# Kernel tuning notes

Hardware: AMD Instinct MI355X
Metric: run time of the kernel (lower is better)

## Reference

```python
import jax, jax.numpy as jnp
import numpy as np

jax.config.update("jax_enable_x64", True)  # FixedPointMul math is done in float64, as in torch

B, S, H = 8, 4096, 768


def setup_inputs():
    key = jax.random.key(0)
    k = jax.random.split(key, 6)
    s_act = jnp.array([4.0 / 127.0], dtype=jnp.float32)  # per-tensor 8-bit activation scale

    def qact(kk):  # produce int8-quantized-looking activations
        x = jax.random.normal(kk, (B, S, H), jnp.float32)
        return s_act * jnp.clip(jnp.round(x / s_act), -128, 127)

    return {
        "hidden_states": qact(k[0]),
        "hidden_states_scaling_factor": s_act,
        "input_tensor": qact(k[1]),
        "input_tensor_scaling_factor": s_act,
        "dense_weight": 0.02 * jax.random.normal(k[2], (H, H), jnp.float32),
        "dense_bias": 0.01 * jax.random.normal(k[3], (H,), jnp.float32),
        "ln_weight": 1.0 + 0.05 * jax.random.normal(k[4], (H,), jnp.float32),
        "ln_bias": 0.05 * jax.random.normal(k[5], (H,), jnp.float32),
    }


def _sym_scale(k, smin, smax):
    n = 2 ** (k - 1) - 1
    return jnp.clip(jnp.maximum(jnp.abs(smin), jnp.abs(smax)), 1e-8, None) / n


def _sym_quant(x, k, scale):
    n = 2 ** (k - 1) - 1
    return jnp.clip(jnp.round(x / scale), -n, n - 1)


def _batch_frexp(x):
    # returns (round(mantissa * 2^31), 31 - exponent) as in ibert batch_frexp
    m, e = jnp.frexp(x)
    return jnp.floor(m * (2.0 ** 31) + 0.5), 31.0 - e


def _fixedpoint_mul(x, pre_scale, bit, z_scale, identity=None, id_scale=None):
    n = 2 ** (bit - 1) - 1
    ps = jnp.reshape(pre_scale, (1, 1, -1)).astype(jnp.float64)
    z = z_scale.astype(jnp.float64)
    z_int = jnp.round(x.astype(jnp.float64) / ps)
    m, e = _batch_frexp(ps / z)
    out = jnp.round(z_int * m / (2.0 ** e))
    if identity is not None:
        isf = jnp.reshape(id_scale, (1, 1, -1)).astype(jnp.float64)
        wx = jnp.round(identity.astype(jnp.float64) / isf)
        m1, e1 = _batch_frexp(isf / z)
        out = out + jnp.round(wx * m1 / (2.0 ** e1))
    return jnp.clip(out, -n - 1, n).astype(jnp.float32)


def _quant_act(x, bit, pre_scale, identity=None, id_scale=None):
    x_act = x if identity is None else x + identity
    s = _sym_scale(bit, x_act.min(), x_act.max())  # per-tensor scale (dynamic range)
    q = _fixedpoint_mul(x, pre_scale, bit, s, identity, id_scale)
    return q * s, s


def reference(hidden_states, hidden_states_scaling_factor, input_tensor, input_tensor_scaling_factor, dense_weight, dense_bias, ln_weight, ln_bias):
    # ---- QuantLinear: per-channel int8 weights, int32 bias ----
    w_min = dense_weight.min(axis=1)
    w_max = dense_weight.max(axis=1)
    fc_scale = _sym_scale(8, w_min, w_max)                      # [H_out]
    w_int = _sym_quant(dense_weight, 8, fc_scale[:, None])      # [H_out, H_in]
    bias_scale = fc_scale * hidden_states_scaling_factor        # [H_out]
    b_int = _sym_quant(dense_bias, 32, bias_scale)
    x_int = hidden_states / hidden_states_scaling_factor
    hs = (jnp.einsum("bsh,oh->bso", x_int, w_int) + b_int) * bias_scale
    # dropout: eval mode -> identity
    # ---- QuantAct(22-bit) with quantized residual add ----
    hs, ln_in_scale = _quant_act(hs, 22, bias_scale, input_tensor, input_tensor_scaling_factor)
    # ---- IntLayerNorm (integer-only LayerNorm) ----
    x_int = hs / ln_in_scale
    mean_int = jnp.round(jnp.mean(x_int, axis=2, keepdims=True))
    y_int = x_int - mean_int
    var0 = jnp.sum(y_int ** 2, axis=2, keepdims=True)
    shift = jnp.ceil(jnp.log2(jnp.sqrt(jnp.maximum(var0, 1.0) / 2.0 ** 32)))  # set_shift (max_bit=32)
    shift = jnp.maximum(0.0, shift.max())
    y_sh = jnp.floor(y_int / 2.0 ** shift)
    var_int = jnp.sum(y_sh ** 2, axis=2, keepdims=True)
    std_int = jnp.floor(jnp.sqrt(var_int)) * 2.0 ** shift
    factor = jnp.floor(2.0 ** 31 / std_int)
    y_int = jnp.floor(y_int * factor / 2.0)
    sf = jnp.sqrt(jnp.float32(H)) / 2.0 ** 30
    bias_int = jnp.floor((ln_bias / ln_weight) / sf)
    y_int = y_int + bias_int
    sf_out = sf * ln_weight                                     # [H]
    hs = y_int * sf_out
    # ---- QuantAct(8-bit) output requantization ----
    hs, out_scale = _quant_act(hs, 8, sf_out)
    return hs, out_scale
```

## Files before the change

kernel.cpp:

```cpp
#include <hip/hip_runtime.h>

typedef int   v4i   __attribute__((ext_vector_type(4)));
typedef unsigned long u64x2 __attribute__((ext_vector_type(2)));

#define HDIM 768
#define NTOK 32768

static constexpr size_t WX_OFF   = 0;
static constexpr size_t WINT_OFF = 25165824;
static constexpr size_t FACT_OFF = WINT_OFF + 589824;
static constexpr size_t RS1_OFF  = WINT_OFF + 1179648;
static constexpr size_t RS2_OFF  = RS1_OFF + 6144;
static constexpr size_t BS_OFF   = RS2_OFF + 6144;
static constexpr size_t BINT_OFF = BS_OFF + 3072;
static constexpr size_t LNBI_OFF = BINT_OFF + 3072;
static constexpr size_t SFO_OFF  = LNBI_OFF + 3072;
static constexpr size_t SC_OFF   = SFO_OFF + 3072;
static constexpr size_t RSM1_OFF = SC_OFF + 64;
static constexpr size_t INP8_OFF = RSM1_OFF + 64;
static constexpr size_t WS_NEED8 = INP8_OFF + (size_t)NTOK * HDIM;

__device__ __forceinline__ unsigned fenc(float f) {
    unsigned u = __float_as_uint(f);
    return (u >> 31) ? ~u : (u | 0x80000000u);
}
__device__ __forceinline__ float fdec(unsigned e) {
    unsigned u = (e >> 31) ? (e & 0x7fffffffu) : ~e;
    return __uint_as_float(u);
}

#define GLDS16(g, l) __builtin_amdgcn_global_load_lds( \
    (const __attribute__((address_space(1))) unsigned int*)(g), \
    (__attribute__((address_space(3))) unsigned int*)(l), 16, 0, 0)

__device__ __forceinline__ int swz4(int r) { return (r & 3) ^ ((r >> 2) & 3); }

__global__ __launch_bounds__(256) void k0_prep(const float* __restrict__ W,
                                               const float* __restrict__ bias,
                                               const float* __restrict__ ln_w,
                                               const float* __restrict__ ln_b,
                                               const float* __restrict__ phsf,
                                               char* __restrict__ ws) {
    int o = blockIdx.x, tid = threadIdx.x;
    __shared__ float red[256];
    __shared__ float fc_sh;
    float m = 0.f;
    for (int j = tid; j < HDIM; j += 256) m = fmaxf(m, fabsf(W[(size_t)o * HDIM + j]));
    red[tid] = m;
    __syncthreads();
    for (int s = 128; s; s >>= 1) { if (tid < s) red[tid] = fmaxf(red[tid], red[tid + s]); __syncthreads(); }
    if (tid == 0) {
        float fc = fmaxf(red[0], 1e-8f) / 127.0f;
        float hsf = *phsf;
        float bs = fc * hsf;
        fc_sh = fc;
        ((float*)(ws + BS_OFF))[o] = bs;
        ((int*)(ws + BINT_OFF))[o] = (int)rintf(bias[o] / bs);
        float sf = sqrtf(768.0f) / 1073741824.0f;
        float lw = ln_w[o], lb = ln_b[o];
        ((int*)(ws + LNBI_OFF))[o] = (int)floorf((lb / lw) / sf);
        ((float*)(ws + SFO_OFF))[o] = sf * lw;
    }
    __syncthreads();
    float fc = fc_sh;
    char* w8 = (char*)(ws + WINT_OFF);
    for (int j = tid; j < HDIM; j += 256) {
        float q = rintf(W[(size_t)o * HDIM + j] / fc);
        q = fminf(fmaxf(q, -127.f), 126.f);
        w8[(size_t)o * HDIM + j] = (char)q;
    }
    if (blockIdx.x == 0 && tid < 8) {
        unsigned* sc = (unsigned*)(ws + SC_OFF);
        unsigned v = 0u;
        if (tid == 0 || tid == 2) v = 0xFFFFFFFFu;
        sc[tid] = v;
    }
}

__global__ __launch_bounds__(256) void kp_a8(const float* __restrict__ hs,
                                             const float* __restrict__ phsf,
                                             char* __restrict__ ws) {
    int tid = threadIdx.x;
    size_t b4 = (size_t)blockIdx.x * 1024 + tid;
    float inv = 1.0f / *phsf;
    const float4* in4 = (const float4*)hs;
    unsigned* o32 = (unsigned*)(ws + WX_OFF);
    #pragma unroll
    for (int j = 0; j < 4; ++j) {
        float4 v = in4[b4 + j * 256];
        int q0 = (int)rintf(v.x * inv), q1 = (int)rintf(v.y * inv);
        int q2 = (int)rintf(v.z * inv), q3 = (int)rintf(v.w * inv);
        o32[b4 + j * 256] = (unsigned)(q0 & 255) | ((unsigned)(q1 & 255) << 8) |
                            ((unsigned)(q2 & 255) << 16) | ((unsigned)(q3 & 255) << 24);
    }
}

#define BM 128
#define BN 192
#define BK 64
#define NKT (HDIM / BK)
#define SROW 196
template<int U8>
__global__ __launch_bounds__(256) void k1_gemm(const float* __restrict__ inp,
                                               char* __restrict__ i8,
                                               const float* __restrict__ pisf,
                                               char* __restrict__ ws,
                                               int* __restrict__ accOut) {
    __shared__ alignas(16) char smem[40992];
    char* As0 = smem;
    char* Bs0 = smem + 16384;
    float* rmn = (float*)(smem + 40960);
    float* rmx = rmn + 4;
    int tid = threadIdx.x, lane = tid & 63, wave = tid >> 6;
    int wrow = lane & 15, g = lane >> 4;
    int bid = blockIdx.x;
    int xcd = bid & 7, slot = bid >> 3;
    int mtile = xcd * 32 + (slot >> 2);
    int ntile = slot & 3;
    int t0 = mtile * BM, o0 = ntile * BN;
    const char* a8 = (const char*)(ws + WX_OFF);
    const char* w8 = (const char*)(ws + WINT_OFF);

    const char* asrc[2]; const char* bsrc[3];
    int aldso[2], bldso[3];
    #pragma unroll
    for (int i = 0; i < 2; ++i) {
        int c = i * 256 + tid, r = c >> 2, s = c & 3;
        asrc[i] = a8 + (size_t)(t0 + r) * HDIM + (s ^ swz4(r)) * 16;
        aldso[i] = (i * 256 + wave * 64) * 16;
    }
    #pragma unroll
    for (int i = 0; i < 3; ++i) {
        int c = i * 256 + tid, r = c >> 2, s = c & 3;
        bsrc[i] = w8 + (size_t)(o0 + r) * HDIM + (s ^ swz4(r)) * 16;
        bldso[i] = (i * 256 + wave * 64) * 16;
    }

    int wm = wave & 1, wn = wave >> 1;
    int aofs[4], bofs[6];
    #pragma unroll
    for (int mi = 0; mi < 4; ++mi) { int r = wm * 64 + mi * 16 + wrow; aofs[mi] = r * BK + ((g ^ swz4(r)) * 16); }
    #pragma unroll
    for (int nf = 0; nf < 6; ++nf) { int r = wn * 96 + nf * 16 + wrow; bofs[nf] = r * BK + ((g ^ swz4(r)) * 16); }

    #pragma unroll
    for (int i = 0; i < 2; ++i) GLDS16(asrc[i], As0 + aldso[i]);
    #pragma unroll
    for (int i = 0; i < 3; ++i) GLDS16(bsrc[i], Bs0 + bldso[i]);
    #pragma unroll
    for (int i = 0; i < 2; ++i) GLDS16(asrc[i] + BK, As0 + 8192 + aldso[i]);
    #pragma unroll
    for (int i = 0; i < 3; ++i) GLDS16(bsrc[i] + BK, Bs0 + 12288 + bldso[i]);
    asm volatile("s_waitcnt vmcnt(5)" ::: "memory");
    __builtin_amdgcn_s_barrier();

    v4i acc[4][6] = {};
    for (int kt = 0; kt < NKT; ++kt) {
        int cur = kt & 1;
        const char* Ac = As0 + cur * 8192;
        const char* Bc = Bs0 + cur * 12288;
        u64x2 af[4], bf[6];
        #pragma unroll
        for (int mi = 0; mi < 4; ++mi) af[mi] = *(const u64x2*)(Ac + aofs[mi]);
        #pragma unroll
        for (int nf = 0; nf < 6; ++nf) bf[nf] = *(const u64x2*)(Bc + bofs[nf]);
        asm volatile("s_waitcnt lgkmcnt(0)" ::: "memory");
        __builtin_amdgcn_s_barrier();
        if (kt + 2 < NKT) {
            #pragma unroll
            for (int i = 0; i < 2; ++i) GLDS16(asrc[i] + (kt + 2) * BK, As0 + cur * 8192 + aldso[i]);
            #pragma unroll
            for (int i = 0; i < 3; ++i) GLDS16(bsrc[i] + (kt + 2) * BK, Bs0 + cur * 12288 + bldso[i]);
        }
        __builtin_amdgcn_s_setprio(1);
        #pragma unroll
        for (int mi = 0; mi < 4; ++mi)
            #pragma unroll
            for (int nf = 0; nf < 6; ++nf) {
                acc[mi][nf] = __builtin_amdgcn_mfma_i32_16x16x32_i8((long)af[mi][0], (long)bf[nf][0], acc[mi][nf], 0, 0, 0);
                acc[mi][nf] = __builtin_amdgcn_mfma_i32_16x16x32_i8((long)af[mi][1], (long)bf[nf][1], acc[mi][nf], 0, 0, 0);
            }
        __builtin_amdgcn_s_setprio(0);
        if (kt + 2 < NKT) {
            asm volatile("s_waitcnt vmcnt(5)" ::: "memory");
            __builtin_amdgcn_s_barrier();
        } else if (kt + 2 == NKT) {
            asm volatile("s_waitcnt vmcnt(0)" ::: "memory");
            __builtin_amdgcn_s_barrier();
        }
    }

    const float* bscale = (const float*)(ws + BS_OFF);
    const int* bint = (const int*)(ws + BINT_OFF);
    float inv_isf = U8 ? (1.0f / *pisf) : 0.f;
    int* sAcc = (int*)smem;
    float lmn = 3.402823466e38f, lmx = -3.402823466e38f;
    #pragma unroll
    for (int mi = 0; mi < 4; ++mi) {
        __syncthreads();
        #pragma unroll
        for (int nf = 0; nf < 6; ++nf)
            #pragma unroll
            for (int r = 0; r < 4; ++r)
                sAcc[(wm * 16 + g * 4 + r) * SROW + wn * 96 + nf * 16 + wrow] = acc[mi][nf][r];
        __syncthreads();
        #pragma unroll
        for (int k = 0; k < 6; ++k) {
            int i4 = tid + k * 256;
            int sr = i4 / 48, c4 = i4 - sr * 48;
            int t = t0 + (sr >> 4) * 64 + mi * 16 + (sr & 15);
            int col = o0 + c4 * 4;
            int4 a4 = *(const int4*)&sAcc[sr * SROW + c4 * 4];
            int4 b4 = *(const int4*)&bint[col];
            float4 bs4 = *(const float4*)&bscale[col];
            a4.x += b4.x; a4.y += b4.y; a4.z += b4.z; a4.w += b4.w;
            size_t idx = (size_t)t * HDIM + col;
            *(int4*)&accOut[idx] = a4;
            float4 x4 = *(const float4*)&inp[idx];
            if (U8) {
                int w0 = (int)rintf(x4.x * inv_isf), w1 = (int)rintf(x4.y * inv_isf);
                int w2 = (int)rintf(x4.z * inv_isf), w3 = (int)rintf(x4.w * inv_isf);
                *(unsigned*)(i8 + idx) = (unsigned)(w0 & 255) | ((unsigned)(w1 & 255) << 8) |
                                         ((unsigned)(w2 & 255) << 16) | ((unsigned)(w3 & 255) << 24);
            }
            float xa;
            xa = (float)a4.x * bs4.x + x4.x; lmn = fminf(lmn, xa); lmx = fmaxf(lmx, xa);
            xa = (float)a4.y * bs4.y + x4.y; lmn = fminf(lmn, xa); lmx = fmaxf(lmx, xa);
            xa = (float)a4.z * bs4.z + x4.z; lmn = fminf(lmn, xa); lmx = fmaxf(lmx, xa);
            xa = (float)a4.w * bs4.w + x4.w; lmn = fminf(lmn, xa); lmx = fmaxf(lmx, xa);
        }
    }
    #pragma unroll
    for (int off = 32; off; off >>= 1) {
        lmn = fminf(lmn, __shfl_down(lmn, off));
        lmx = fmaxf(lmx, __shfl_down(lmx, off));
    }
    __syncthreads();
    if (lane == 0) { rmn[wave] = lmn; rmx[wave] = lmx; }
    __syncthreads();
    if (tid == 0) {
        float mn = fminf(fminf(rmn[0], rmn[1]), fminf(rmn[2], rmn[3]));
        float mx = fmaxf(fmaxf(rmx[0], rmx[1]), fmaxf(rmx[2], rmx[3]));
        volatile unsigned* sc = (volatile unsigned*)(ws + SC_OFF);
        unsigned emn = fenc(mn), emx = fenc(mx);
        if (emn < sc[0]) atomicMin((unsigned*)&sc[0], emn);
        if (emx > sc[1]) atomicMax((unsigned*)&sc[1], emx);
    }
}

__global__ __launch_bounds__(256) void k2_scale1(const float* __restrict__ pisf, char* __restrict__ ws) {
    __shared__ float s_sh;
    unsigned* sc = (unsigned*)(ws + SC_OFF);
    if (threadIdx.x == 0) {
        float mn = fdec(sc[0]), mx = fdec(sc[1]);
        float s = fmaxf(fmaxf(fabsf(mn), fabsf(mx)), 1e-8f) / 2097151.0f;
        ((float*)sc)[5] = s;
        s_sh = s;
        double r = (double)(*pisf) / (double)s;
        int ex; double mant = frexp(r, &ex);
        double m1 = floor(mant * 2147483648.0 + 0.5);
        ((double*)(ws + RSM1_OFF))[0] = m1 * exp2((double)(ex - 31));
    }
    __syncthreads();
    float s = s_sh;
    const float* bs = (const float*)(ws + BS_OFF);
    double* rs1 = (double*)(ws + RS1_OFF);
    for (int o = threadIdx.x; o < HDIM; o += 256) {
        double r = (double)bs[o] / (double)s;
        int ex; double mant = frexp(r, &ex);
        double m = floor(mant * 2147483648.0 + 0.5);
        rs1[o] = m * exp2((double)(ex - 31));
    }
}

template<int U8>
__global__ __launch_bounds__(256) void k3_rows(char* __restrict__ ws, int* __restrict__ buf,
                                               const float* __restrict__ inp,
                                               const char* __restrict__ i8,
                                               const float* __restrict__ pisf) {
    int tid = threadIdx.x, lane = tid & 63, wave = tid >> 6;
    int wid = blockIdx.x * 4 + wave;
    const double* rs1 = (const double*)(ws + RS1_OFF);
    double rsm1 = *(const double*)(ws + RSM1_OFF);
    float inv_isf = 1.0f / *pisf;
    double t_rs1[12];
    #pragma unroll
    for (int c = 0; c < 3; ++c) {
        int o0 = (lane + 64 * c) * 4;
        #pragma unroll
        for (int j = 0; j < 4; ++j) t_rs1[c * 4 + j] = rs1[o0 + j];
    }
    int localShift = 0;
    int4 aP[3]; float4 xP[3]; int wP[3];
    {
        size_t b0 = (size_t)(wid * 4) * HDIM;
        #pragma unroll
        for (int c = 0; c < 3; ++c) {
            aP[c] = ((const int4*)(buf + b0))[lane + 64 * c];
            if (U8) wP[c] = ((const int*)(i8 + b0))[lane + 64 * c];
            else    xP[c] = ((const float4*)(inp + b0))[lane + 64 * c];
        }
    }
    for (int rr = 0; rr < 4; ++rr) {
        int4 aN[3]; float4 xN[3]; int wN[3];
        if (rr < 3) {
            size_t nb = (size_t)(wid * 4 + rr + 1) * HDIM;
            #pragma unroll
            for (int c = 0; c < 3; ++c) {
                aN[c] = ((const int4*)(buf + nb))[lane + 64 * c];
                if (U8) wN[c] = ((const int*)(i8 + nb))[lane + 64 * c];
                else    xN[c] = ((const float4*)(inp + nb))[lane + 64 * c];
            }
        }
        size_t base = (size_t)(wid * 4 + rr) * HDIM;
        int q[12];
        int sum = 0;
        #pragma unroll
        for (int c = 0; c < 3; ++c) {
            int av[4] = {aP[c].x, aP[c].y, aP[c].z, aP[c].w};
            #pragma unroll
            for (int j = 0; j < 4; ++j) {
                double q1 = rint((double)av[j] * t_rs1[c * 4 + j]);
                int wxj;
                if (U8) wxj = (int)(char)(wP[c] >> (8 * j));
                else {
                    float xv = (j == 0) ? xP[c].x : (j == 1) ? xP[c].y : (j == 2) ? xP[c].z : xP[c].w;
                    wxj = (int)rintf(xv * inv_isf);
                }
                double qq = q1 + rint((double)wxj * rsm1);
                qq = fmin(fmax(qq, -2097152.0), 2097151.0);
                q[c * 4 + j] = (int)qq;
                sum += q[c * 4 + j];
            }
        }
        #pragma unroll
        for (int off = 32; off; off >>= 1) sum += __shfl_xor(sum, off);
        int mean = (int)rint((double)sum / 768.0);
        long long var0 = 0;
        #pragma unroll
        for (int k = 0; k < 12; ++k) { q[k] -= mean; var0 += (long long)q[k] * (long long)q[k]; }
        #pragma unroll
        for (int off = 32; off; off >>= 1) var0 += __shfl_xor(var0, off);
        #pragma unroll
        for (int c = 0; c < 3; ++c) {
            int4 y = {q[c * 4 + 0], q[c * 4 + 1], q[c * 4 + 2], q[c * 4 + 3]};
            ((int4*)(buf + base))[lane + 64 * c] = y;
        }
        if (lane == 0) {
            double v = (double)(var0 < 1 ? 1LL : var0);
            int sr = (int)ceil(0.5 * log2(v) - 16.0);
            localShift = max(localShift, sr);
        }
        #pragma unroll
        for (int c = 0; c < 3; ++c) { aP[c] = aN[c]; xP[c] = xN[c]; wP[c] = wN[c]; }
    }
    if (lane == 0 && localShift > 0) {
        int* sp = (int*)(ws + SC_OFF) + 4;
        if (localShift > *(volatile int*)sp) atomicMax(sp, localShift);
    }
}

__global__ __launch_bounds__(256) void k4_rows(char* __restrict__ ws, const int* __restrict__ buf) {
    int tid = threadIdx.x, lane = tid & 63, wave = tid >> 6;
    int wid = blockIdx.x * 4 + wave;
    int shift = *(((const int*)(ws + SC_OFF)) + 4);
    const int* lnbi = (const int*)(ws + LNBI_OFF);
    const float* sfo = (const float*)(ws + SFO_OFF);
    __shared__ float rmn[4], rmx[4];
    int t_lnbi[12]; float t_sfo[12];
    #pragma unroll
    for (int c = 0; c < 3; ++c) {
        int o0 = (lane + 64 * c) * 4;
        #pragma unroll
        for (int j = 0; j < 4; ++j) { t_lnbi[c * 4 + j] = lnbi[o0 + j]; t_sfo[c * 4 + j] = sfo[o0 + j]; }
    }
    unsigned* fact = (unsigned*)(ws + FACT_OFF);
    float lmn = 3.402823466e38f, lmx = -3.402823466e38f;
    int4 yP[3];
    {
        size_t b0 = (size_t)(wid * 4) * HDIM;
        #pragma unroll
        for (int c = 0; c < 3; ++c) yP[c] = ((const int4*)(buf + b0))[lane + 64 * c];
    }
    for (int rr = 0; rr < 4; ++rr) {
        int4 yN[3];
        if (rr < 3) {
            size_t nb = (size_t)(wid * 4 + rr + 1) * HDIM;
            #pragma unroll
            for (int c = 0; c < 3; ++c) yN[c] = ((const int4*)(buf + nb))[lane + 64 * c];
        }
        int yv[12];
        #pragma unroll
        for (int c = 0; c < 3; ++c) {
            yv[c * 4 + 0] = yP[c].x; yv[c * 4 + 1] = yP[c].y; yv[c * 4 + 2] = yP[c].z; yv[c * 4 + 3] = yP[c].w;
        }
        long long var = 0;
        #pragma unroll
        for (int k = 0; k < 12; ++k) { int ysh = yv[k] >> shift; var += (long long)ysh * (long long)ysh; }
        #pragma unroll
        for (int off = 32; off; off >>= 1) var += __shfl_xor(var, off);
        double std_int = floor(sqrt((double)var)) * (double)(1LL << shift);
        if (std_int < 1.0) std_int = 1.0;
        long long factor = (long long)floor(2147483648.0 / std_int);
        if (lane == 0) fact[wid * 4 + rr] = (unsigned)factor;
        #pragma unroll
        for (int k = 0; k < 12; ++k) {
            long long t = ((long long)yv[k] * factor) >> 1;
            int v2 = (int)t + t_lnbi[k];
            float h = (float)v2 * t_sfo[k];
            lmn = fminf(lmn, h);
            lmx = fmaxf(lmx, h);
        }
        #pragma unroll
        for (int c = 0; c < 3; ++c) yP[c] = yN[c];
    }
    #pragma unroll
    for (int off = 32; off; off >>= 1) {
        lmn = fminf(lmn, __shfl_xor(lmn, off));
        lmx = fmaxf(lmx, __shfl_xor(lmx, off));
    }
    if (lane == 0) { rmn[wave] = lmn; rmx[wave] = lmx; }
    __syncthreads();
    if (tid == 0) {
        float mn = fminf(fminf(rmn[0], rmn[1]), fminf(rmn[2], rmn[3]));
        float mx = fmaxf(fmaxf(rmx[0], rmx[1]), fmaxf(rmx[2], rmx[3]));
        volatile unsigned* sc = (volatile unsigned*)(ws + SC_OFF);
        unsigned emn = fenc(mn), emx = fenc(mx);
        if (emn < sc[2]) atomicMin((unsigned*)&sc[2], emn);
        if (emx > sc[3]) atomicMax((unsigned*)&sc[3], emx);
    }
}

__global__ __launch_bounds__(256) void k5_scale2(char* __restrict__ ws) {
    __shared__ float s_sh;
    unsigned* sc = (unsigned*)(ws + SC_OFF);
    if (threadIdx.x == 0) {
        float mn = fdec(sc[2]), mx = fdec(sc[3]);
        float s2 = fmaxf(fmaxf(fabsf(mn), fabsf(mx)), 1e-8f) / 127.0f;
        ((float*)sc)[6] = s2;
        s_sh = s2;
    }
    __syncthreads();
    float s2 = s_sh;
    const float* sfo = (const float*)(ws + SFO_OFF);
    double* rs2 = (double*)(ws + RS2_OFF);
    for (int o = threadIdx.x; o < HDIM; o += 256) {
        double r = (double)sfo[o] / (double)s2;
        int ex; double mant = frexp(r, &ex);
        double m = floor(mant * 2147483648.0 + 0.5);
        rs2[o] = m * exp2((double)(ex - 31));
    }
}

__global__ __launch_bounds__(256) void k6_out(char* __restrict__ ws, float* __restrict__ out) {
    int tid = threadIdx.x, lane = tid & 63, wave = tid >> 6;
    int wid = blockIdx.x * 4 + wave;
    const double* rs2 = (const double*)(ws + RS2_OFF);
    const int* lnbi = (const int*)(ws + LNBI_OFF);
    const unsigned* fact = (const unsigned*)(ws + FACT_OFF);
    float s2 = ((const float*)(ws + SC_OFF))[6];
    double t_rs2[12]; int t_lnbi[12];
    #pragma unroll
    for (int c = 0; c < 3; ++c) {
        int o0 = (lane + 64 * c) * 4;
        #pragma unroll
        for (int j = 0; j < 4; ++j) { t_rs2[c * 4 + j] = rs2[o0 + j]; t_lnbi[c * 4 + j] = lnbi[o0 + j]; }
    }
    int* buf = (int*)out;
    int4 yP[3];
    {
        size_t b0 = (size_t)(wid * 4) * HDIM;
        #pragma unroll
        for (int c = 0; c < 3; ++c) yP[c] = ((const int4*)(buf + b0))[lane + 64 * c];
    }
    for (int rr = 0; rr < 4; ++rr) {
        int4 yN[3];
        if (rr < 3) {
            size_t nb = (size_t)(wid * 4 + rr + 1) * HDIM;
            #pragma unroll
            for (int c = 0; c < 3; ++c) yN[c] = ((const int4*)(buf + nb))[lane + 64 * c];
        }
        size_t base = (size_t)(wid * 4 + rr) * HDIM;
        long long factor = (long long)fact[wid * 4 + rr];
        int yv[12];
        #pragma unroll
        for (int c = 0; c < 3; ++c) {
            yv[c * 4 + 0] = yP[c].x; yv[c * 4 + 1] = yP[c].y; yv[c * 4 + 2] = yP[c].z; yv[c * 4 + 3] = yP[c].w;
        }
        #pragma unroll
        for (int c = 0; c < 3; ++c) {
            float4 r;
            float* rp = &r.x;
            #pragma unroll
            for (int j = 0; j < 4; ++j) {
                int k = c * 4 + j;
                long long t = ((long long)yv[k] * factor) >> 1;
                int v2 = (int)t + t_lnbi[k];
                double q = rint((double)v2 * t_rs2[k]);
                q = fmin(fmax(q, -128.0), 127.0);
                rp[j] = (float)q * s2;
            }
            ((float4*)(out + base))[lane + 64 * c] = r;
        }
        #pragma unroll
        for (int c = 0; c < 3; ++c) yP[c] = yN[c];
    }
    if (wid == 0 && tid == 0) out[(size_t)NTOK * HDIM] = s2;
}

extern "C" void kernel_launch(void* const* d_in, const int* in_sizes, int n_in,
                              void* d_out, int out_size, void* d_ws, size_t ws_size,
                              hipStream_t stream) {
    const float* hs   = (const float*)d_in[0];
    const float* phsf = (const float*)d_in[1];
    const float* inp  = (const float*)d_in[2];
    const float* pisf = (const float*)d_in[3];
    const float* W    = (const float*)d_in[4];
    const float* bias = (const float*)d_in[5];
    const float* ln_w = (const float*)d_in[6];
    const float* ln_b = (const float*)d_in[7];
    char* ws = (char*)d_ws;
    float* out = (float*)d_out;
    int* buf = (int*)d_out;
    char* i8 = ws + INP8_OFF;
    bool use8 = ws_size >= WS_NEED8;

    k0_prep<<<HDIM, 256, 0, stream>>>(W, bias, ln_w, ln_b, phsf, ws);
    kp_a8<<<NTOK * HDIM / 4096, 256, 0, stream>>>(hs, phsf, ws);
    if (use8) {
        k1_gemm<1><<<(NTOK / BM) * (HDIM / BN), 256, 0, stream>>>(inp, i8, pisf, ws, buf);
        k2_scale1<<<1, 256, 0, stream>>>(pisf, ws);
        k3_rows<1><<<NTOK / 16, 256, 0, stream>>>(ws, buf, inp, i8, pisf);
    } else {
        k1_gemm<0><<<(NTOK / BM) * (HDIM / BN), 256, 0, stream>>>(inp, i8, pisf, ws, buf);
        k2_scale1<<<1, 256, 0, stream>>>(pisf, ws);
        k3_rows<0><<<NTOK / 16, 256, 0, stream>>>(ws, buf, inp, i8, pisf);
    }
    k4_rows<<<NTOK / 16, 256, 0, stream>>>(ws, buf);
    k5_scale2<<<1, 256, 0, stream>>>(ws);
    k6_out<<<NTOK / 16, 256, 0, stream>>>(ws, out);
}
```

Baseline: 431.5 us.

## Shrink GEMM N-tile to 128 and pre-quantize residual input in separate pass

The GEMM tile changes from 128x192 to 128x128, giving six N-tiles per M-tile, less shared memory, and launch bounds of 3 blocks per CU for higher occupancy. Quantizing the residual input to int8 moves from the GEMM epilogue into a new standalone kernel, and the epilogue now reads the int8 residual and dequantizes it instead of reading fp32. This adds a full extra pass over the fp32 input but cuts epilogue traffic and register pressure. The smaller tile also re-reads the activation tile more often across N-tiles.

```diff
diff --git a/kernel.cpp b/kernel.cpp
--- a/kernel.cpp
+++ b/kernel.cpp
@@ -95,94 +95,107 @@
     }
 }
 
+__global__ __launch_bounds__(256) void kp_i8(const float* __restrict__ inp,
+                                             const float* __restrict__ pisf,
+                                             char* __restrict__ ws) {
+    int tid = threadIdx.x;
+    size_t b4 = (size_t)blockIdx.x * 1024 + tid;
+    float inv = 1.0f / *pisf;
+    const float4* in4 = (const float4*)inp;
+    unsigned* o32 = (unsigned*)(ws + INP8_OFF);
+    #pragma unroll
+    for (int j = 0; j < 4; ++j) {
+        float4 v = in4[b4 + j * 256];
+        int q0 = (int)rintf(v.x * inv), q1 = (int)rintf(v.y * inv);
+        int q2 = (int)rintf(v.z * inv), q3 = (int)rintf(v.w * inv);
+        o32[b4 + j * 256] = (unsigned)(q0 & 255) | ((unsigned)(q1 & 255) << 8) |
+                            ((unsigned)(q2 & 255) << 16) | ((unsigned)(q3 & 255) << 24);
+    }
+}
+
 #define BM 128
-#define BN 192
+#define BN 128
 #define BK 64
 #define NKT (HDIM / BK)
-#define SROW 196
+#define SROW 132
 template<int U8>
-__global__ __launch_bounds__(256) void k1_gemm(const float* __restrict__ inp,
-                                               char* __restrict__ i8,
-                                               const float* __restrict__ pisf,
-                                               char* __restrict__ ws,
-                                               int* __restrict__ accOut) {
-    __shared__ alignas(16) char smem[40992];
+__global__ __launch_bounds__(256, 3) void k1_gemm(const float* __restrict__ inp,
+                                                  const char* __restrict__ i8,
+                                                  const float* __restrict__ pisf,
+                                                  char* __restrict__ ws,
+                                                  int* __restrict__ accOut) {
+    __shared__ alignas(16) char smem[32800];
     char* As0 = smem;
     char* Bs0 = smem + 16384;
-    float* rmn = (float*)(smem + 40960);
+    float* rmn = (float*)(smem + 32768);
     float* rmx = rmn + 4;
     int tid = threadIdx.x, lane = tid & 63, wave = tid >> 6;
     int wrow = lane & 15, g = lane >> 4;
     int bid = blockIdx.x;
     int xcd = bid & 7, slot = bid >> 3;
-    int mtile = xcd * 32 + (slot >> 2);
-    int ntile = slot & 3;
+    int mtile = xcd * 32 + slot / 6;
+    int ntile = slot % 6;
     int t0 = mtile * BM, o0 = ntile * BN;
     const char* a8 = (const char*)(ws + WX_OFF);
     const char* w8 = (const char*)(ws + WINT_OFF);
 
-    const char* asrc[2]; const char* bsrc[3];
-    int aldso[2], bldso[3];
+    const char* asrc[2]; const char* bsrc[2];
+    int ldso[2];
     #pragma unroll
     for (int i = 0; i < 2; ++i) {
         int c = i * 256 + tid, r = c >> 2, s = c & 3;
         asrc[i] = a8 + (size_t)(t0 + r) * HDIM + (s ^ swz4(r)) * 16;
-        aldso[i] = (i * 256 + wave * 64) * 16;
-    }
-    #pragma unroll
-    for (int i = 0; i < 3; ++i) {
-        int c = i * 256 + tid, r = c >> 2, s = c & 3;
         bsrc[i] = w8 + (size_t)(o0 + r) * HDIM + (s ^ swz4(r)) * 16;
-        bldso[i] = (i * 256 + wave * 64) * 16;
+        ldso[i] = (i * 256 + wave * 64) * 16;
     }
 
     int wm = wave & 1, wn = wave >> 1;
-    int aofs[4], bofs[6];
+    int aofs[4], bofs[4];
     #pragma unroll
     for (int mi = 0; mi < 4; ++mi) { int r = wm * 64 + mi * 16 + wrow; aofs[mi] = r * BK + ((g ^ swz4(r)) * 16); }
     #pragma unroll
-    for (int nf = 0; nf < 6; ++nf) { int r = wn * 96 + nf * 16 + wrow; bofs[nf] = r * BK + ((g ^ swz4(r)) * 16); }
-
-    #pragma unroll
-    for (int i = 0; i < 2; ++i) GLDS16(asrc[i], As0 + aldso[i]);
-    #pragma unroll
-    for (int i = 0; i < 3; ++i) GLDS16(bsrc[i], Bs0 + bldso[i]);
-    #pragma unroll
-    for (int i = 0; i < 2; ++i) GLDS16(asrc[i] + BK, As0 + 8192 + aldso[i]);
-    #pragma unroll
-    for (int i = 0; i < 3; ++i) GLDS16(bsrc[i] + BK, Bs0 + 12288 + bldso[i]);
-    asm volatile("s_waitcnt vmcnt(5)" ::: "memory");
+    for (int nf = 0; nf < 4; ++nf) { int r = wn * 64 + nf * 16 + wrow; bofs[nf] = r * BK + ((g ^ swz4(r)) * 16); }
+
+    #pragma unroll
+    for (int i = 0; i < 2; ++i) GLDS16(asrc[i], As0 + ldso[i]);
+    #pragma unroll
+    for (int i = 0; i < 2; ++i) GLDS16(bsrc[i], Bs0 + ldso[i]);
+    #pragma unroll
+    for (int i = 0; i < 2; ++i) GLDS16(asrc[i] + BK, As0 + 8192 + ldso[i]);
+    #pragma unroll
+    for (int i = 0; i < 2; ++i) GLDS16(bsrc[i] + BK, Bs0 + 8192 + ldso[i]);
+    asm volatile("s_waitcnt vmcnt(4)" ::: "memory");
     __builtin_amdgcn_s_barrier();
 
-    v4i acc[4][6] = {};
+    v4i acc[4][4] = {};
     for (int kt = 0; kt < NKT; ++kt) {
         int cur = kt & 1;
         const char* Ac = As0 + cur * 8192;
-        const char* Bc = Bs0 + cur * 12288;
-        u64x2 af[4], bf[6];
+        const char* Bc = Bs0 + cur * 8192;
+        u64x2 af[4], bf[4];
         #pragma unroll
         for (int mi = 0; mi < 4; ++mi) af[mi] = *(const u64x2*)(Ac + aofs[mi]);
         #pragma unroll
-        for (int nf = 0; nf < 6; ++nf) bf[nf] = *(const u64x2*)(Bc + bofs[nf]);
+        for (int nf = 0; nf < 4; ++nf) bf[nf] = *(const u64x2*)(Bc + bofs[nf]);
         asm volatile("s_waitcnt lgkmcnt(0)" ::: "memory");
         __builtin_amdgcn_s_barrier();
         if (kt + 2 < NKT) {
             #pragma unroll
-            for (int i = 0; i < 2; ++i) GLDS16(asrc[i] + (kt + 2) * BK, As0 + cur * 8192 + aldso[i]);
-            #pragma unroll
-            for (int i = 0; i < 3; ++i) GLDS16(bsrc[i] + (kt + 2) * BK, Bs0 + cur * 12288 + bldso[i]);
+            for (int i = 0; i < 2; ++i) GLDS16(asrc[i] + (kt + 2) * BK, As0 + cur * 8192 + ldso[i]);
+            #pragma unroll
+            for (int i = 0; i < 2; ++i) GLDS16(bsrc[i] + (kt + 2) * BK, Bs0 + cur * 8192 + ldso[i]);
         }
         __builtin_amdgcn_s_setprio(1);
         #pragma unroll
         for (int mi = 0; mi < 4; ++mi)
             #pragma unroll
-            for (int nf = 0; nf < 6; ++nf) {
+            for (int nf = 0; nf < 4; ++nf) {
                 acc[mi][nf] = __builtin_amdgcn_mfma_i32_16x16x32_i8((long)af[mi][0], (long)bf[nf][0], acc[mi][nf], 0, 0, 0);
                 acc[mi][nf] = __builtin_amdgcn_mfma_i32_16x16x32_i8((long)af[mi][1], (long)bf[nf][1], acc[mi][nf], 0, 0, 0);
             }
         __builtin_amdgcn_s_setprio(0);
         if (kt + 2 < NKT) {
-            asm volatile("s_waitcnt vmcnt(5)" ::: "memory");
+            asm volatile("s_waitcnt vmcnt(4)" ::: "memory");
             __builtin_amdgcn_s_barrier();
         } else if (kt + 2 == NKT) {
             asm volatile("s_waitcnt vmcnt(0)" ::: "memory");
@@ -192,22 +205,22 @@
 
     const float* bscale = (const float*)(ws + BS_OFF);
     const int* bint = (const int*)(ws + BINT_OFF);
-    float inv_isf = U8 ? (1.0f / *pisf) : 0.f;
+    float isf = U8 ? *pisf : 0.f;
     int* sAcc = (int*)smem;
     float lmn = 3.402823466e38f, lmx = -3.402823466e38f;
     #pragma unroll
     for (int mi = 0; mi < 4; ++mi) {
         __syncthreads();
         #pragma unroll
-        for (int nf = 0; nf < 6; ++nf)
+        for (int nf = 0; nf < 4; ++nf)
             #pragma unroll
             for (int r = 0; r < 4; ++r)
-                sAcc[(wm * 16 + g * 4 + r) * SROW + wn * 96 + nf * 16 + wrow] = acc[mi][nf][r];
+                sAcc[(wm * 16 + g * 4 + r) * SROW + wn * 64 + nf * 16 + wrow] = acc[mi][nf][r];
         __syncthreads();
         #pragma unroll
-        for (int k = 0; k < 6; ++k) {
+        for (int k = 0; k < 4; ++k) {
             int i4 = tid + k * 256;
-            int sr = i4 / 48, c4 = i4 - sr * 48;
+            int sr = i4 >> 5, c4 = i4 & 31;
             int t = t0 + (sr >> 4) * 64 + mi * 16 + (sr & 15);
             int col = o0 + c4 * 4;
             int4 a4 = *(const int4*)&sAcc[sr * SROW + c4 * 4];
@@ -216,18 +229,22 @@
             a4.x += b4.x; a4.y += b4.y; a4.z += b4.z; a4.w += b4.w;
             size_t idx = (size_t)t * HDIM + col;
             *(int4*)&accOut[idx] = a4;
-            float4 x4 = *(const float4*)&inp[idx];
+            float x0, x1, x2, x3;
             if (U8) {
-                int w0 = (int)rintf(x4.x * inv_isf), w1 = (int)rintf(x4.y * inv_isf);
-                int w2 = (int)rintf(x4.z * inv_isf), w3 = (int)rintf(x4.w * inv_isf);
-                *(unsigned*)(i8 + idx) = (unsigned)(w0 & 255) | ((unsigned)(w1 & 255) << 8) |
-                                         ((unsigned)(w2 & 255) << 16) | ((unsigned)(w3 & 255) << 24);
+                unsigned w = *(const unsigned*)(i8 + idx);
+                x0 = (float)(int)(char)(w) * isf;
+                x1 = (float)(int)(char)(w >> 8) * isf;
+                x2 = (float)(int)(char)(w >> 16) * isf;
+                x3 = (float)(int)(char)(w >> 24) * isf;
+            } else {
+                float4 x4 = *(const float4*)&inp[idx];
+                x0 = x4.x; x1 = x4.y; x2 = x4.z; x3 = x4.w;
             }
             float xa;
-            xa = (float)a4.x * bs4.x + x4.x; lmn = fminf(lmn, xa); lmx = fmaxf(lmx, xa);
-            xa = (float)a4.y * bs4.y + x4.y; lmn = fminf(lmn, xa); lmx = fmaxf(lmx, xa);
-            xa = (float)a4.z * bs4.z + x4.z; lmn = fminf(lmn, xa); lmx = fmaxf(lmx, xa);
-            xa = (float)a4.w * bs4.w + x4.w; lmn = fminf(lmn, xa); lmx = fmaxf(lmx, xa);
+            xa = (float)a4.x * bs4.x + x0; lmn = fminf(lmn, xa); lmx = fmaxf(lmx, xa);
+            xa = (float)a4.y * bs4.y + x1; lmn = fminf(lmn, xa); lmx = fmaxf(lmx, xa);
+            xa = (float)a4.z * bs4.z + x2; lmn = fminf(lmn, xa); lmx = fmaxf(lmx, xa);
+            xa = (float)a4.w * bs4.w + x3; lmn = fminf(lmn, xa); lmx = fmaxf(lmx, xa);
         }
     }
     #pragma unroll
@@ -522,12 +539,13 @@
     char* ws = (char*)d_ws;
     float* out = (float*)d_out;
     int* buf = (int*)d_out;
-    char* i8 = ws + INP8_OFF;
+    const char* i8 = (const char*)(ws + INP8_OFF);
     bool use8 = ws_size >= WS_NEED8;
 
     k0_prep<<<HDIM, 256, 0, stream>>>(W, bias, ln_w, ln_b, phsf, ws);
     kp_a8<<<NTOK * HDIM / 4096, 256, 0, stream>>>(hs, phsf, ws);
     if (use8) {
+        kp_i8<<<NTOK * HDIM / 4096, 256, 0, stream>>>(inp, pisf, ws);
         k1_gemm<1><<<(NTOK / BM) * (HDIM / BN), 256, 0, stream>>>(inp, i8, pisf, ws, buf);
         k2_scale1<<<1, 256, 0, stream>>>(pisf, ws);
         k3_rows<1><<<NTOK / 16, 256, 0, stream>>>(ws, buf, inp, i8, pisf);
```

Result: no change. 432.4 us (+0.2%).
